# Optimization experiments

Hardware: AMD Instinct MI355X
Metric: run time of the kernel (lower is better)

## Reference

```python
import jax, jax.numpy as jnp
import numpy as np

NEG_INF = -1e10  # matches torch -10000000000.0


def setup_inputs() -> dict:
    key = jax.random.key(0)
    ks = jax.random.split(key, 8)
    L, B, E, H, HID, A = 2048, 32, 512, 512, 512, 512
    input_data = jax.random.normal(ks[0], (L, B, E), dtype=jnp.float32)
    mask = jax.random.randint(ks[1], (L, B), 0, 2, dtype=jnp.int32)
    action_feature = jax.random.normal(ks[2], (B, A), dtype=jnp.float32)
    hidden_state = jax.random.normal(ks[3], (B, H), dtype=jnp.float32)
    state = jax.random.normal(ks[4], (B, H), dtype=jnp.float32)
    W1 = jax.random.normal(ks[5], (H + E, HID), dtype=jnp.float32) * (1.0 / np.sqrt(H + E))
    b1 = jnp.zeros((HID,), dtype=jnp.float32)
    W2 = jax.random.normal(ks[6], (HID, 1), dtype=jnp.float32) * (1.0 / np.sqrt(HID))
    b2 = jnp.zeros((1,), dtype=jnp.float32)
    return {"input_data": input_data, "mask": mask, "action_feature": action_feature,
            "hidden_state": hidden_state, "state": state,
            "W1": W1, "b1": b1, "W2": W2, "b2": b2}


def reference(input_data, mask, action_feature, hidden_state, state, W1, b1, W2, b2):
    # input_data: (L, B, E); hidden_state: (B, H)
    H = hidden_state.shape[-1]
    # query = concat([hidden broadcast over L, input_data], -1); split W1 to avoid
    # materializing the (L, B, H+E) concat.
    W1_h, W1_e = W1[:H], W1[H:]                      # (H, HID), (E, HID)
    pre = hidden_state @ W1_h + b1                   # (B, HID)
    pre = pre[None] + jnp.einsum('lbe,eh->lbh', input_data, W1_e)  # (L, B, HID)
    logit = (jnp.tanh(pre) @ W2).squeeze(-1) + b2[0]  # (L, B)
    logit = jnp.where(mask != 0, logit, NEG_INF)
    p = jax.nn.softmax(logit, axis=0)                 # softmax over L
    ctx = jnp.einsum('lbe,lb->be', input_data, p)     # (B, E)
    return jnp.concatenate([ctx, action_feature], axis=1)
```

## Files before the change

kernel.cpp:

```cpp
#include <hip/hip_runtime.h>
#include <hip/hip_bf16.h>
#include <stdint.h>

#define L_DIM 2048
#define B_DIM 32
#define E_DIM 512
#define HID_DIM 512
#define M_DIM (L_DIM * B_DIM)

typedef float f32x4 __attribute__((ext_vector_type(4)));
typedef short bf16x8 __attribute__((ext_vector_type(8)));

#define OFF_BASE  0
#define OFF_WT    65536
#define OFF_LOGIT 589824
#define OFF_P     851968
#define OFF_PART  1114112

__device__ __forceinline__ unsigned short f2bf(float f) {
  unsigned int u = __float_as_uint(f);
  u = (u + 0x7FFFu + ((u >> 16) & 1u)) >> 16;
  return (unsigned short)u;
}

__device__ __forceinline__ float tanh_fast(float x) {
  float xc = fminf(fmaxf(x, -15.f), 15.f);
  float e = __expf(2.f * xc);
  return (e - 1.f) * __builtin_amdgcn_rcpf(e + 1.f);
}

__device__ __forceinline__ uint4 pack8(const float4& a, const float4& b) {
  uint4 r;
  r.x = (unsigned)f2bf(a.x) | ((unsigned)f2bf(a.y) << 16);
  r.y = (unsigned)f2bf(a.z) | ((unsigned)f2bf(a.w) << 16);
  r.z = (unsigned)f2bf(b.x) | ((unsigned)f2bf(b.y) << 16);
  r.w = (unsigned)f2bf(b.z) | ((unsigned)f2bf(b.w) << 16);
  return r;
}

__global__ __launch_bounds__(256) void k_base(const float* __restrict__ hidden,
                                              const float* __restrict__ W1,
                                              const float* __restrict__ b1,
                                              float* __restrict__ base) {
  const int b = blockIdx.x;
  const int tid = threadIdx.x;
  __shared__ float hs[HID_DIM];
  {
    float2 v = *(const float2*)(hidden + (size_t)b * 512 + tid * 2);
    hs[tid * 2] = v.x; hs[tid * 2 + 1] = v.y;
  }
  __syncthreads();
  const int h = tid * 2;
  float2 b1v = *(const float2*)(b1 + h);
  float ax = b1v.x, ay = b1v.y;
#pragma unroll 8
  for (int e = 0; e < 512; ++e) {
    float2 w = *(const float2*)(W1 + (size_t)e * 512 + h);
    float hv = hs[e];
    ax = fmaf(hv, w.x, ax);
    ay = fmaf(hv, w.y, ay);
  }
  float2 r; r.x = ax; r.y = ay;
  *(float2*)(base + (size_t)b * 512 + h) = r;
}

__global__ __launch_bounds__(256) void k_prep_wt(const float* __restrict__ W1,
                                                 unsigned short* __restrict__ Wt) {
  const int kc = blockIdx.x;
  const int tid = threadIdx.x;
  __shared__ unsigned short sh[32][516];
#pragma unroll
  for (int i = 0; i < 16; ++i) {
    int f4 = i * 256 + tid;
    int r = f4 >> 7;
    int c = (f4 & 127) * 4;
    float4 v = *(const float4*)(W1 + (size_t)(512 + kc * 32 + r) * 512 + c);
    sh[r][c + 0] = f2bf(v.x); sh[r][c + 1] = f2bf(v.y);
    sh[r][c + 2] = f2bf(v.z); sh[r][c + 3] = f2bf(v.w);
  }
  __syncthreads();
#pragma unroll
  for (int i = 0; i < 8; ++i) {
    int u = i * 256 + tid;
    int n = ((u >> 9) << 7) + (((u >> 6) & 7) << 4) + (u & 15);
    int k0 = ((u >> 4) & 3) << 3;
    alignas(16) unsigned short tmp[8];
#pragma unroll
    for (int j = 0; j < 8; ++j) tmp[j] = sh[k0 + j][n];
    *(uint4*)(Wt + ((size_t)kc * 2048 + u) * 8) = *(const uint4*)tmp;
  }
}

__global__ __launch_bounds__(512, 2) void k_logits(
    const float* __restrict__ x, const unsigned short* __restrict__ Wt,
    const float* __restrict__ base, const float* __restrict__ W2,
    float* __restrict__ logit) {
  __shared__ unsigned short xs[32768];
  const int tid = threadIdx.x;
  const int m0 = blockIdx.x * 64;
  const int w = tid >> 6, lane = tid & 63;
  const int lg = lane >> 4, l15 = lane & 15;

  {
    const int r = (tid & 7) + w * 8;
    const int j = (tid >> 3) & 7;
    const float* xrow = x + (size_t)(m0 + r) * 512;
    const int ubase = ((r >> 4) << 6) + (r & 15);
    float4 va[8], vb[8];
#pragma unroll
    for (int i = 0; i < 8; ++i) {
      int s = i * 8 + j;
      va[i] = *(const float4*)(xrow + s * 8);
      vb[i] = *(const float4*)(xrow + s * 8 + 4);
    }
#pragma unroll
    for (int i = 0; i < 8; ++i) {
      int s = i * 8 + j;
      int u = ((s >> 2) << 8) + ((s & 3) << 4) + ubase;
      *(uint4*)(&xs[u * 8]) = pack8(va[i], vb[i]);
    }
  }
  __syncthreads();

  int ub[4];
#pragma unroll
  for (int ni = 0; ni < 4; ++ni) {
    int nb = w * 64 + ni * 16;
    ub[ni] = ((nb >> 7) << 9) + (((nb >> 4) & 7) << 6);
  }

  f32x4 acc[4][4];
#pragma unroll
  for (int mi = 0; mi < 4; ++mi)
#pragma unroll
    for (int ni = 0; ni < 4; ++ni) acc[mi][ni] = (f32x4){0.f, 0.f, 0.f, 0.f};

#pragma unroll 4
  for (int kc = 0; kc < 16; ++kc) {
    uint4 bw[4];
    const uint4* bsrc = (const uint4*)Wt + (size_t)kc * 2048;
#pragma unroll
    for (int ni = 0; ni < 4; ++ni) bw[ni] = bsrc[ub[ni] + lane];
    bf16x8 af[4];
#pragma unroll
    for (int mi = 0; mi < 4; ++mi)
      af[mi] = *(const bf16x8*)(&xs[(kc * 256 + mi * 64 + lane) * 8]);
#pragma unroll
    for (int mi = 0; mi < 4; ++mi)
#pragma unroll
      for (int ni = 0; ni < 4; ++ni)
        acc[mi][ni] = __builtin_amdgcn_mfma_f32_16x16x32_bf16(
            af[mi], *(const bf16x8*)(&bw[ni]), acc[mi][ni], 0, 0, 0);
  }

  float w2v[4];
#pragma unroll
  for (int ni = 0; ni < 4; ++ni) w2v[ni] = W2[w * 64 + ni * 16 + l15];
  float lsum[4][4];
#pragma unroll
  for (int mi = 0; mi < 4; ++mi) {
#pragma unroll
    for (int rg = 0; rg < 4; ++rg) {
      int m = m0 + mi * 16 + lg * 4 + rg;
      int bb = m & 31;
      const float* brow = base + (size_t)bb * 512 + w * 64;
      float s = 0.f;
#pragma unroll
      for (int ni = 0; ni < 4; ++ni) {
        float pre = acc[mi][ni][rg] + brow[ni * 16 + l15];
        s = fmaf(tanh_fast(pre), w2v[ni], s);
      }
      lsum[mi][rg] = s;
    }
  }
  __syncthreads();
  float (*lred)[64] = (float (*)[64])xs;
#pragma unroll
  for (int mi = 0; mi < 4; ++mi)
#pragma unroll
    for (int rg = 0; rg < 4; ++rg) {
      float v = lsum[mi][rg];
      v += __shfl_xor(v, 1); v += __shfl_xor(v, 2);
      v += __shfl_xor(v, 4); v += __shfl_xor(v, 8);
      if (l15 == 0) lred[w][mi * 16 + lg * 4 + rg] = v;
    }
  __syncthreads();
  if (tid < 64) {
    float v = 0.f;
#pragma unroll
    for (int wq = 0; wq < 8; ++wq) v += lred[wq][tid];
    logit[m0 + tid] = v;
  }
}

__global__ __launch_bounds__(256) void k_softmax(const float* __restrict__ logit,
                                                 const int* __restrict__ mask,
                                                 float* __restrict__ p) {
  const int b = blockIdx.x, tid = threadIdx.x;
  float lv[8]; float mx = -3.0e38f;
#pragma unroll
  for (int i = 0; i < 8; ++i) {
    int idx = (tid + i * 256) * 32 + b;
    float v = (mask[idx] != 0) ? logit[idx] : -1.0e10f;
    lv[i] = v; mx = fmaxf(mx, v);
  }
  __shared__ float red[8];
  for (int d = 1; d < 64; d <<= 1) mx = fmaxf(mx, __shfl_xor(mx, d));
  if ((tid & 63) == 0) red[tid >> 6] = mx;
  __syncthreads();
  mx = fmaxf(fmaxf(red[0], red[1]), fmaxf(red[2], red[3]));
  float s = 0.f;
#pragma unroll
  for (int i = 0; i < 8; ++i) { lv[i] = __expf(lv[i] - mx); s += lv[i]; }
  for (int d = 1; d < 64; d <<= 1) s += __shfl_xor(s, d);
  __syncthreads();
  if ((tid & 63) == 0) red[4 + (tid >> 6)] = s;
  __syncthreads();
  s = (red[4] + red[5]) + (red[6] + red[7]);
  float inv = 1.f / s;
#pragma unroll
  for (int i = 0; i < 8; ++i) {
    int idx = (tid + i * 256) * 32 + b;
    p[idx] = lv[i] * inv;
  }
}

__global__ __launch_bounds__(128) void k_ctx(const float* __restrict__ x,
                                             const float* __restrict__ p,
                                             float* __restrict__ part) {
  const int blk = blockIdx.x;
  const int b = blk >> 5, ch = blk & 31;
  const int tid = threadIdx.x;
  __shared__ float ps[64];
  const int l0 = ch * 64;
  if (tid < 64) ps[tid] = p[(l0 + tid) * 32 + b];
  __syncthreads();
  const float* xb = x + ((size_t)l0 * 32 + b) * 512 + tid * 4;
  float ax = 0.f, ay = 0.f, az = 0.f, aw = 0.f;
#pragma unroll 4
  for (int i = 0; i < 64; ++i) {
    float4 v = *(const float4*)(xb + (size_t)i * 32 * 512);
    float pv = ps[i];
    ax = fmaf(pv, v.x, ax); ay = fmaf(pv, v.y, ay);
    az = fmaf(pv, v.z, az); aw = fmaf(pv, v.w, aw);
  }
  float4 r; r.x = ax; r.y = ay; r.z = az; r.w = aw;
  *(float4*)(part + (size_t)blk * 512 + tid * 4) = r;
}

__global__ __launch_bounds__(256) void k_final(const float* __restrict__ part,
                                               const float* __restrict__ af,
                                               float* __restrict__ out) {
  const int b = blockIdx.x, tid = threadIdx.x;
  float ax = 0.f, ay = 0.f;
#pragma unroll
  for (int ch = 0; ch < 32; ++ch) {
    float2 v = *(const float2*)(part + ((size_t)(b * 32 + ch) * 512) + tid * 2);
    ax += v.x; ay += v.y;
  }
  float2 r; r.x = ax; r.y = ay;
  *(float2*)(out + (size_t)b * 1024 + tid * 2) = r;
  float2 a = *(const float2*)(af + (size_t)b * 512 + tid * 2);
  *(float2*)(out + (size_t)b * 1024 + 512 + tid * 2) = a;
}

extern "C" void kernel_launch(void* const* d_in, const int* in_sizes, int n_in,
                              void* d_out, int out_size, void* d_ws, size_t ws_size,
                              hipStream_t stream) {
  const float* x      = (const float*)d_in[0];
  const int*   mask   = (const int*)d_in[1];
  const float* af     = (const float*)d_in[2];
  const float* hidden = (const float*)d_in[3];
  const float* W1     = (const float*)d_in[5];
  const float* b1     = (const float*)d_in[6];
  const float* W2     = (const float*)d_in[7];
  float* out = (float*)d_out;
  char* ws = (char*)d_ws;
  float*          base  = (float*)(ws + OFF_BASE);
  unsigned short* Wt    = (unsigned short*)(ws + OFF_WT);
  float*          logit = (float*)(ws + OFF_LOGIT);
  float*          p     = (float*)(ws + OFF_P);
  float*          part  = (float*)(ws + OFF_PART);

  k_base   <<<32,   256, 0, stream>>>(hidden, W1, b1, base);
  k_prep_wt<<<16,   256, 0, stream>>>(W1, Wt);
  k_logits <<<1024, 512, 0, stream>>>(x, Wt, base, W2, logit);
  k_softmax<<<32,   256, 0, stream>>>(logit, mask, p);
  k_ctx    <<<1024, 128, 0, stream>>>(x, p, part);
  k_final  <<<32,   256, 0, stream>>>(part, af, out);
}
```

Before: 112.0 us.

## Split N into halves with double-buffered asm weight loads and raise occupancy

Restructures the k_logits GEMM so each wave handles the N dimension in two passes of 32 columns, holding half as many accumulators. This lowers register pressure, allowing launch bounds of 4 blocks per CU. Weight fragments are loaded with inline-asm global loads into a double buffer with explicit vmcnt waits, and MFMA phases are wrapped in s_setprio, to overlap global-load latency with matrix math. It risks correctness fragility from manual waitcnt handling. LDS use of 64KB per block may also cap the occupancy the new bound asks for.

```diff
diff --git a/kernel.cpp b/kernel.cpp
--- a/kernel.cpp
+++ b/kernel.cpp
@@ -10,6 +10,7 @@
 
 typedef float f32x4 __attribute__((ext_vector_type(4)));
 typedef short bf16x8 __attribute__((ext_vector_type(8)));
+typedef unsigned int u32x4 __attribute__((ext_vector_type(4)));
 
 #define OFF_BASE  0
 #define OFF_WT    65536
@@ -37,6 +38,14 @@
   r.w = (unsigned)f2bf(b.z) | ((unsigned)f2bf(b.w) << 16);
   return r;
 }
+
+#define GLX4(dst, voff, sbase) \
+  asm volatile("global_load_dwordx4 %0, %1, %2" \
+               : "=v"(dst) : "v"(voff), "s"(sbase))
+#define VMWAIT2 do { asm volatile("s_waitcnt vmcnt(2)" ::: "memory"); \
+                     __builtin_amdgcn_sched_barrier(0); } while (0)
+#define VMWAIT0 do { asm volatile("s_waitcnt vmcnt(0)" ::: "memory"); \
+                     __builtin_amdgcn_sched_barrier(0); } while (0)
 
 __global__ __launch_bounds__(256) void k_base(const float* __restrict__ hidden,
                                               const float* __restrict__ W1,
@@ -91,7 +100,7 @@
   }
 }
 
-__global__ __launch_bounds__(512, 2) void k_logits(
+__global__ __launch_bounds__(512, 4) void k_logits(
     const float* __restrict__ x, const unsigned short* __restrict__ Wt,
     const float* __restrict__ base, const float* __restrict__ W2,
     float* __restrict__ logit) {
@@ -122,57 +131,110 @@
   }
   __syncthreads();
 
-  int ub[4];
-#pragma unroll
-  for (int ni = 0; ni < 4; ++ni) {
-    int nb = w * 64 + ni * 16;
-    ub[ni] = ((nb >> 7) << 9) + (((nb >> 4) & 7) << 6);
-  }
-
-  f32x4 acc[4][4];
+  float lsum[4][4];
 #pragma unroll
   for (int mi = 0; mi < 4; ++mi)
 #pragma unroll
-    for (int ni = 0; ni < 4; ++ni) acc[mi][ni] = (f32x4){0.f, 0.f, 0.f, 0.f};
-
-#pragma unroll 4
-  for (int kc = 0; kc < 16; ++kc) {
-    uint4 bw[4];
-    const uint4* bsrc = (const uint4*)Wt + (size_t)kc * 2048;
-#pragma unroll
-    for (int ni = 0; ni < 4; ++ni) bw[ni] = bsrc[ub[ni] + lane];
-    bf16x8 af[4];
+    for (int rg = 0; rg < 4; ++rg) lsum[mi][rg] = 0.f;
+
+#pragma unroll 1
+  for (int nh = 0; nh < 2; ++nh) {
+    const int nb0 = nh * 256 + w * 32;
+    const int nb1 = nb0 + 16;
+    unsigned vo0 = (((nb0 >> 7) << 9) + (((nb0 >> 4) & 7) << 6) + lane) * 16u;
+    unsigned vo1 = (((nb1 >> 7) << 9) + (((nb1 >> 4) & 7) << 6) + lane) * 16u;
+
+    f32x4 acc[4][2];
 #pragma unroll
     for (int mi = 0; mi < 4; ++mi)
-      af[mi] = *(const bf16x8*)(&xs[(kc * 256 + mi * 64 + lane) * 8]);
-#pragma unroll
-    for (int mi = 0; mi < 4; ++mi)
-#pragma unroll
-      for (int ni = 0; ni < 4; ++ni)
-        acc[mi][ni] = __builtin_amdgcn_mfma_f32_16x16x32_bf16(
-            af[mi], *(const bf16x8*)(&bw[ni]), acc[mi][ni], 0, 0, 0);
-  }
-
-  float w2v[4];
-#pragma unroll
-  for (int ni = 0; ni < 4; ++ni) w2v[ni] = W2[w * 64 + ni * 16 + l15];
-  float lsum[4][4];
-#pragma unroll
-  for (int mi = 0; mi < 4; ++mi) {
-#pragma unroll
-    for (int rg = 0; rg < 4; ++rg) {
-      int m = m0 + mi * 16 + lg * 4 + rg;
-      int bb = m & 31;
-      const float* brow = base + (size_t)bb * 512 + w * 64;
-      float s = 0.f;
-#pragma unroll
-      for (int ni = 0; ni < 4; ++ni) {
-        float pre = acc[mi][ni][rg] + brow[ni * 16 + l15];
-        s = fmaf(tanh_fast(pre), w2v[ni], s);
-      }
-      lsum[mi][rg] = s;
-    }
-  }
+#pragma unroll
+      for (int ni = 0; ni < 2; ++ni) acc[mi][ni] = (f32x4){0.f, 0.f, 0.f, 0.f};
+
+    u32x4 b0a, b0b, b1a, b1b;
+    GLX4(b0a, vo0, Wt); GLX4(b0b, vo1, Wt); vo0 += 32768u; vo1 += 32768u;
+
+#pragma unroll 1
+    for (int kc2 = 0; kc2 < 7; ++kc2) {
+      const int k0 = kc2 * 2;
+      GLX4(b1a, vo0, Wt); GLX4(b1b, vo1, Wt); vo0 += 32768u; vo1 += 32768u;
+      bf16x8 af[4];
+#pragma unroll
+      for (int mi = 0; mi < 4; ++mi)
+        af[mi] = *(const bf16x8*)(&xs[(k0 * 256 + mi * 64 + lane) * 8]);
+      VMWAIT2;
+      __builtin_amdgcn_s_setprio(1);
+#pragma unroll
+      for (int mi = 0; mi < 4; ++mi) {
+        acc[mi][0] = __builtin_amdgcn_mfma_f32_16x16x32_bf16(
+            af[mi], *(const bf16x8*)(&b0a), acc[mi][0], 0, 0, 0);
+        acc[mi][1] = __builtin_amdgcn_mfma_f32_16x16x32_bf16(
+            af[mi], *(const bf16x8*)(&b0b), acc[mi][1], 0, 0, 0);
+      }
+      __builtin_amdgcn_s_setprio(0);
+      GLX4(b0a, vo0, Wt); GLX4(b0b, vo1, Wt); vo0 += 32768u; vo1 += 32768u;
+      bf16x8 ag[4];
+#pragma unroll
+      for (int mi = 0; mi < 4; ++mi)
+        ag[mi] = *(const bf16x8*)(&xs[((k0 + 1) * 256 + mi * 64 + lane) * 8]);
+      VMWAIT2;
+      __builtin_amdgcn_s_setprio(1);
+#pragma unroll
+      for (int mi = 0; mi < 4; ++mi) {
+        acc[mi][0] = __builtin_amdgcn_mfma_f32_16x16x32_bf16(
+            ag[mi], *(const bf16x8*)(&b1a), acc[mi][0], 0, 0, 0);
+        acc[mi][1] = __builtin_amdgcn_mfma_f32_16x16x32_bf16(
+            ag[mi], *(const bf16x8*)(&b1b), acc[mi][1], 0, 0, 0);
+      }
+      __builtin_amdgcn_s_setprio(0);
+    }
+    {
+      GLX4(b1a, vo0, Wt); GLX4(b1b, vo1, Wt);
+      bf16x8 af[4];
+#pragma unroll
+      for (int mi = 0; mi < 4; ++mi)
+        af[mi] = *(const bf16x8*)(&xs[(14 * 256 + mi * 64 + lane) * 8]);
+      VMWAIT2;
+#pragma unroll
+      for (int mi = 0; mi < 4; ++mi) {
+        acc[mi][0] = __builtin_amdgcn_mfma_f32_16x16x32_bf16(
+            af[mi], *(const bf16x8*)(&b0a), acc[mi][0], 0, 0, 0);
+        acc[mi][1] = __builtin_amdgcn_mfma_f32_16x16x32_bf16(
+            af[mi], *(const bf16x8*)(&b0b), acc[mi][1], 0, 0, 0);
+      }
+      bf16x8 ag[4];
+#pragma unroll
+      for (int mi = 0; mi < 4; ++mi)
+        ag[mi] = *(const bf16x8*)(&xs[(15 * 256 + mi * 64 + lane) * 8]);
+      VMWAIT0;
+#pragma unroll
+      for (int mi = 0; mi < 4; ++mi) {
+        acc[mi][0] = __builtin_amdgcn_mfma_f32_16x16x32_bf16(
+            ag[mi], *(const bf16x8*)(&b1a), acc[mi][0], 0, 0, 0);
+        acc[mi][1] = __builtin_amdgcn_mfma_f32_16x16x32_bf16(
+            ag[mi], *(const bf16x8*)(&b1b), acc[mi][1], 0, 0, 0);
+      }
+    }
+    unsigned long long bpi = (unsigned long long)base;
+    unsigned long long wpi = (unsigned long long)W2;
+    asm volatile("" : "+s"(bpi), "+s"(wpi));
+    const float* bp = (const float*)bpi;
+    const float* wp = (const float*)wpi;
+    const float w2v0 = wp[nb0 + l15];
+    const float w2v1 = wp[nb1 + l15];
+#pragma unroll
+    for (int mi = 0; mi < 4; ++mi) {
+#pragma unroll
+      for (int rg = 0; rg < 4; ++rg) {
+        int m = m0 + mi * 16 + lg * 4 + rg;
+        int bb = m & 31;
+        const float* brow = bp + (size_t)bb * 512 + nb0;
+        float pre0 = acc[mi][0][rg] + brow[l15];
+        float pre1 = acc[mi][1][rg] + brow[16 + l15];
+        lsum[mi][rg] += tanh_fast(pre0) * w2v0 + tanh_fast(pre1) * w2v1;
+      }
+    }
+  }
+
   __syncthreads();
   float (*lred)[64] = (float (*)[64])xs;
 #pragma unroll
```

New measurement: 113.6 us. About the same (+1.5%).
